# Performance work log

Measured on AMD Instinct MI355X. Metric: run time of the kernel, lower is better.

## Reference

```python
import jax, jax.numpy as jnp
import numpy as np

LEAK = 0.2
EPS = 1e-8


def _mod_conv(x, style, weight):
    # x: [B,C,H,W], style: [B,C], weight: [O,C,k,k]
    b, c, h, w = x.shape
    o, _, k, _ = weight.shape
    # per-sample modulation + demodulation (StyleGAN2 style)
    wmod = weight[None] * (style[:, None, :, None, None] + 1.0)  # [B,O,C,k,k]
    d = jax.lax.rsqrt(jnp.sum(wmod * wmod, axis=(2, 3, 4), keepdims=True) + EPS)
    wmod = wmod * d
    pad = (k - 1) // 2  # same padding for stride=1, dilation=1
    xg = x.reshape(1, b * c, h, w)
    wg = wmod.reshape(b * o, c, k, k)
    y = jax.lax.conv_general_dilated(
        xg, wg, window_strides=(1, 1), padding=[(pad, pad), (pad, pad)],
        dimension_numbers=('NCHW', 'OIHW', 'NCHW'), feature_group_count=b)
    return y.reshape(b, o, h, w)


def setup_inputs() -> dict:
    key = jax.random.key(0)
    ks = jax.random.split(key, 8)
    B, LAT, CIN, F, H, W = 8, 512, 256, 256, 64, 64
    K = 3
    kaiming = lambda k, shape, fan_in: jax.random.normal(k, shape, jnp.float32) * np.sqrt(2.0 / fan_in)
    return {
        'x': jax.random.normal(ks[0], (B, CIN, H, W), jnp.float32),
        'istyle': jax.random.normal(ks[1], (B, LAT), jnp.float32),
        'ws1': jax.random.normal(ks[2], (CIN, LAT), jnp.float32) * (1.0 / np.sqrt(LAT)),
        'bs1': jnp.zeros((CIN,), jnp.float32),
        'conv1_w': kaiming(ks[3], (F, CIN, K, K), CIN * K * K),
        'ws2': jax.random.normal(ks[4], (F, LAT), jnp.float32) * (1.0 / np.sqrt(LAT)),
        'bs2': jnp.zeros((F,), jnp.float32),
        'conv2_w': kaiming(ks[5], (F, F, K, K), F * K * K),
    }


def reference(x, istyle, ws1, bs1, conv1_w, ws2, bs2, conv2_w):
    b, c, h, w = x.shape
    # bilinear upsample x2, align_corners=False (half-pixel centers)
    x = jax.image.resize(x, (b, c, 2 * h, 2 * w), method='bilinear')
    s1 = istyle @ ws1.T + bs1
    x = _mod_conv(x, s1, conv1_w)
    x = jax.nn.leaky_relu(x, LEAK)
    s2 = istyle @ ws2.T + bs2
    x = _mod_conv(x, s2, conv2_w)
    return jax.nn.leaky_relu(x, LEAK)
```

## Files before the change

### kernel.cpp

```cpp
#include <hip/hip_runtime.h>

typedef __bf16 bf16x8 __attribute__((ext_vector_type(8)));
typedef float f32x4 __attribute__((ext_vector_type(4)));


__global__ void style_kernel(const float* __restrict__ istyle,
                             const float* __restrict__ ws1, const float* __restrict__ bs1,
                             const float* __restrict__ ws2, const float* __restrict__ bs2,
                             float* __restrict__ sbuf) {
    int b = blockIdx.x;
    int which = blockIdx.y;
    int c = threadIdx.x;
    const float* ws = which ? ws2 : ws1;
    const float* bs = which ? bs2 : bs1;
    __shared__ float st[512];
    for (int i = threadIdx.x; i < 512; i += 256) st[i] = istyle[b * 512 + i];
    __syncthreads();
    float acc = bs[c];
    const float* wr = ws + (size_t)c * 512;
    for (int l = 0; l < 512; ++l) acc += st[l] * wr[l];
    sbuf[((size_t)which * 8 + b) * 256 + c] = acc;
}

__global__ void modw_kernel(const float* __restrict__ w, const float* __restrict__ s,
                            __bf16* __restrict__ wm) {
    int b = blockIdx.x >> 8;
    int o = blockIdx.x & 255;
    int c = threadIdx.x;
    float sm = s[(size_t)b * 256 + c] + 1.0f;
    float v[9];
    float ss = 0.f;
    const float* wr = w + ((size_t)o * 256 + c) * 9;
#pragma unroll
    for (int t = 0; t < 9; ++t) { v[t] = wr[t] * sm; ss += v[t] * v[t]; }
    __shared__ float red[256];
    red[c] = ss;
    __syncthreads();
    for (int sh = 128; sh > 0; sh >>= 1) {
        if (c < sh) red[c] += red[c + sh];
        __syncthreads();
    }
    float d = rsqrtf(red[0] + 1e-8f);
#pragma unroll
    for (int t = 0; t < 9; ++t)
        wm[(((size_t)(b * 256 + o) * 9 + t) * 256) + c] = (__bf16)(v[t] * d);
}

__global__ void zeropad_kernel(__bf16* __restrict__ xu, __bf16* __restrict__ y1) {
    int p = blockIdx.x;
    int b = blockIdx.y;
    __bf16* buf = blockIdx.z ? y1 : xu;
    int y, x;
    if (p < 130)      { y = 0;           x = p; }
    else if (p < 260) { y = 129;         x = p - 130; }
    else if (p < 388) { y = p - 260 + 1; x = 0; }
    else              { y = p - 388 + 1; x = 129; }
    uint4 z = make_uint4(0, 0, 0, 0);
    *(uint4*)(buf + (((size_t)b * 130 + y) * 130 + x) * 256 + threadIdx.x * 8) = z;
}

__global__ void upsample_kernel(const float* __restrict__ x, __bf16* __restrict__ xu) {
    int ct = blockIdx.x;
    int y  = blockIdx.y;
    int b  = blockIdx.z;
    int c0 = ct * 32;
    __shared__ float up[32 * 132];
    int tid = threadIdx.x;

    int j = y >> 1;
    int y0, y1; float wy0, wy1;
    if (y & 1) { y0 = j; y1 = (j + 1 < 64) ? j + 1 : 63; wy0 = 0.75f; wy1 = 0.25f; }
    else       { y0 = (j - 1 >= 0) ? j - 1 : 0; y1 = j; wy0 = 0.25f; wy1 = 0.75f; }

    int c  = tid >> 3;
    int xs = (tid & 7) * 16;
    const float* row0 = x + ((size_t)(b * 256 + c0 + c) * 64 + y0) * 64;
    const float* row1 = x + ((size_t)(b * 256 + c0 + c) * 64 + y1) * 64;
#pragma unroll
    for (int k = 0; k < 16; ++k) {
        int xo = xs + k;
        int i = xo >> 1;
        int x0, x1; float wx0, wx1;
        if (xo & 1) { x0 = i; x1 = (i + 1 < 64) ? i + 1 : 63; wx0 = 0.75f; wx1 = 0.25f; }
        else        { x0 = (i - 1 >= 0) ? i - 1 : 0; x1 = i; wx0 = 0.25f; wx1 = 0.75f; }
        float v0 = wx0 * row0[x0] + wx1 * row0[x1];
        float v1 = wx0 * row1[x0] + wx1 * row1[x1];
        up[c * 132 + xo] = wy0 * v0 + wy1 * v1;
    }
    __syncthreads();
    int xo = tid >> 1, half = tid & 1;
    union { __bf16 v[8]; uint4 u; } pk;
#pragma unroll
    for (int g = 0; g < 2; ++g) {
#pragma unroll
        for (int i = 0; i < 8; ++i)
            pk.v[i] = (__bf16)up[(half * 16 + g * 8 + i) * 132 + xo];
        *(uint4*)(xu + (((size_t)(b * 130) + y + 1) * 130 + xo + 1) * 256 + c0 + half * 16 + g * 8) = pk.u;
    }
}

template <int PHASE>
__global__ __launch_bounds__(256, 3) void conv_kernel(
    const __bf16* __restrict__ in,
    const __bf16* __restrict__ wm,
    float* __restrict__ outf,
    __bf16* __restrict__ outb) {
    __shared__ __bf16 Al[128 * 64];
    __shared__ __bf16 Bl[128 * 64];
    const int tid   = threadIdx.x;
    const int bid   = blockIdx.x;
    const int swz   = (bid & 7) * 256 + (bid >> 3);
    const int b     = swz >> 8;
    const int bx    = swz & 255;
    const int yrow  = bx >> 1;
    const int mtile = bx & 1;
    const int om    = mtile * 128;
    const int lane  = tid & 63;
    const int wv    = tid >> 6;
    const int wo    = (wv >> 1) * 64;
    const int wn    = (wv & 1) * 64;
    const int lr    = lane >> 3;
    const int lc    = lane & 7;
    const int swzc  = (lc ^ lr) * 8;
    const int arow  = lane & 15;
    const int cgb   = lane >> 4;

    const size_t wmbase = ((size_t)(b * 256 + om + wv * 32 + lr) * 9) * 256 + swzc;
    const size_t inbase = (size_t)b * 130 * 130 * 256 + (size_t)(wv * 32 + lr) * 256 + swzc;

    f32x4 acc[4][4] = {};

    for (int tap = 0; tap < 9; ++tap) {
        const int ky = tap / 3, kx = tap % 3;
        const size_t inrow = inbase + (size_t)((yrow + ky) * 130 + kx) * 256;
        const size_t wrow  = wmbase + (size_t)tap * 256;
        for (int c0 = 0; c0 < 256; c0 += 64) {
#pragma unroll
            for (int q = 0; q < 4; ++q) {
                __builtin_amdgcn_global_load_lds(
                    (const __attribute__((address_space(1))) unsigned int*)(wm + wrow + (size_t)q * 8 * 9 * 256 + c0),
                    (__attribute__((address_space(3))) unsigned int*)(Al + (wv * 32 + q * 8) * 64),
                    16, 0, 0);
                __builtin_amdgcn_global_load_lds(
                    (const __attribute__((address_space(1))) unsigned int*)(in + inrow + (size_t)q * 8 * 256 + c0),
                    (__attribute__((address_space(3))) unsigned int*)(Bl + (wv * 32 + q * 8) * 64),
                    16, 0, 0);
            }
            __syncthreads();
#pragma unroll
            for (int ks = 0; ks < 2; ++ks) {
                const int cg = ks * 4 + cgb;
                bf16x8 af[4], bfr[4];
#pragma unroll
                for (int i = 0; i < 4; ++i) {
                    int ra = wo + i * 16 + arow;
                    af[i]  = *(const bf16x8*)((const char*)Al + ra * 128 + ((cg ^ (ra & 7)) * 16));
                    int rb = wn + i * 16 + arow;
                    bfr[i] = *(const bf16x8*)((const char*)Bl + rb * 128 + ((cg ^ (rb & 7)) * 16));
                }
#pragma unroll
                for (int i = 0; i < 4; ++i)
#pragma unroll
                    for (int j = 0; j < 4; ++j)
                        acc[i][j] = __builtin_amdgcn_mfma_f32_16x16x32_bf16(af[i], bfr[j], acc[i][j], 0, 0, 0);
            }
            __syncthreads();
        }
    }

#pragma unroll
    for (int i = 0; i < 4; ++i) {
#pragma unroll
        for (int j = 0; j < 4; ++j) {
            int o_base = om + wo + i * 16 + (lane >> 4) * 4;
            int n      = wn + j * 16 + (lane & 15);
            if (PHASE == 1) {
                union { __bf16 v[4]; uint2 u; } pk;
#pragma unroll
                for (int r = 0; r < 4; ++r) {
                    float t = acc[i][j][r];
                    t = (t > 0.f) ? t : 0.2f * t;
                    pk.v[r] = (__bf16)t;
                }
                *(uint2*)(outb + (((size_t)(b * 130) + yrow + 1) * 130 + n + 1) * 256 + o_base) = pk.u;
            } else {
#pragma unroll
                for (int r = 0; r < 4; ++r) {
                    float t = acc[i][j][r];
                    t = (t > 0.f) ? t : 0.2f * t;
                    outf[(((size_t)b * 256 + o_base + r) * 128 + yrow) * 128 + n] = t;
                }
            }
        }
    }
}

extern "C" void kernel_launch(void* const* d_in, const int* in_sizes, int n_in,
                              void* d_out, int out_size, void* d_ws, size_t ws_size,
                              hipStream_t stream) {
    const float* x      = (const float*)d_in[0];
    const float* istyle = (const float*)d_in[1];
    const float* ws1    = (const float*)d_in[2];
    const float* bs1    = (const float*)d_in[3];
    const float* w1     = (const float*)d_in[4];
    const float* ws2    = (const float*)d_in[5];
    const float* bs2    = (const float*)d_in[6];
    const float* w2     = (const float*)d_in[7];
    float* out = (float*)d_out;

    char* ws = (char*)d_ws;
    __bf16* xu_p = (__bf16*)(ws);
    __bf16* y1_p = (__bf16*)(ws + 69222400);
    __bf16* wm   = (__bf16*)(ws + 138444800);
    float*  sbuf = (float*)(ws + 147881984);

    style_kernel<<<dim3(8, 2), 256, 0, stream>>>(istyle, ws1, bs1, ws2, bs2, sbuf);
    zeropad_kernel<<<dim3(516, 8, 2), 32, 0, stream>>>(xu_p, y1_p);
    upsample_kernel<<<dim3(8, 128, 8), 256, 0, stream>>>(x, xu_p);
    modw_kernel<<<dim3(2048), 256, 0, stream>>>(w1, sbuf, wm);
    conv_kernel<1><<<dim3(2048), 256, 0, stream>>>(xu_p, wm, nullptr, y1_p);
    modw_kernel<<<dim3(2048), 256, 0, stream>>>(w2, sbuf + 2048, wm);
    conv_kernel<2><<<dim3(2048), 256, 0, stream>>>(y1_p, wm, out, nullptr);
}
```

Baseline: 418.2 us.

## Enlarge conv tile to 256x256 with double-buffered LDS pipeline

Rewrites the modulated-conv implicit GEMM so each 512-thread block computes all 256 output channels over two image rows (256 pixels), instead of 128x128 tiles. Global-to-LDS loads for the next K-step are double-buffered and interleaved with MFMA phases, using explicit vmcnt waits, barriers and setprio. This targets load latency and redundant input/weight traffic across tiles. In exchange it uses 128KB of LDS per block and only 512 blocks, which reduces occupancy and may leave CUs underfilled.

```diff
diff --git a/kernel.cpp b/kernel.cpp
--- a/kernel.cpp
+++ b/kernel.cpp
@@ -3,6 +3,12 @@
 typedef __bf16 bf16x8 __attribute__((ext_vector_type(8)));
 typedef float f32x4 __attribute__((ext_vector_type(4)));
 
+
+#define GLDS(gsrc, ldst) __builtin_amdgcn_global_load_lds( \
+    (const __attribute__((address_space(1))) unsigned int*)(gsrc), \
+    (__attribute__((address_space(3))) unsigned int*)(ldst), 16, 0, 0)
+
+#define MFMA(a, b, c) __builtin_amdgcn_mfma_f32_16x16x32_bf16((a), (b), (c), 0, 0, 0)
 
 __global__ void style_kernel(const float* __restrict__ istyle,
                              const float* __restrict__ ws1, const float* __restrict__ bs1,
@@ -100,95 +106,173 @@
 }
 
 template <int PHASE>
-__global__ __launch_bounds__(256, 3) void conv_kernel(
+__global__ __launch_bounds__(512, 2) void conv_kernel(
     const __bf16* __restrict__ in,
-    const __bf16* __restrict__ wm,
+    const __bf16* __restrict__ wmall,
     float* __restrict__ outf,
     __bf16* __restrict__ outb) {
-    __shared__ __bf16 Al[128 * 64];
-    __shared__ __bf16 Bl[128 * 64];
-    const int tid   = threadIdx.x;
-    const int bid   = blockIdx.x;
-    const int swz   = (bid & 7) * 256 + (bid >> 3);
-    const int b     = swz >> 8;
-    const int bx    = swz & 255;
-    const int yrow  = bx >> 1;
-    const int mtile = bx & 1;
-    const int om    = mtile * 128;
-    const int lane  = tid & 63;
-    const int wv    = tid >> 6;
-    const int wo    = (wv >> 1) * 64;
-    const int wn    = (wv & 1) * 64;
-    const int lr    = lane >> 3;
-    const int lc    = lane & 7;
-    const int swzc  = (lc ^ lr) * 8;
-    const int arow  = lane & 15;
-    const int cgb   = lane >> 4;
-
-    const size_t wmbase = ((size_t)(b * 256 + om + wv * 32 + lr) * 9) * 256 + swzc;
-    const size_t inbase = (size_t)b * 130 * 130 * 256 + (size_t)(wv * 32 + lr) * 256 + swzc;
-
-    f32x4 acc[4][4] = {};
-
-    for (int tap = 0; tap < 9; ++tap) {
-        const int ky = tap / 3, kx = tap % 3;
-        const size_t inrow = inbase + (size_t)((yrow + ky) * 130 + kx) * 256;
-        const size_t wrow  = wmbase + (size_t)tap * 256;
-        for (int c0 = 0; c0 < 256; c0 += 64) {
-#pragma unroll
-            for (int q = 0; q < 4; ++q) {
-                __builtin_amdgcn_global_load_lds(
-                    (const __attribute__((address_space(1))) unsigned int*)(wm + wrow + (size_t)q * 8 * 9 * 256 + c0),
-                    (__attribute__((address_space(3))) unsigned int*)(Al + (wv * 32 + q * 8) * 64),
-                    16, 0, 0);
-                __builtin_amdgcn_global_load_lds(
-                    (const __attribute__((address_space(1))) unsigned int*)(in + inrow + (size_t)q * 8 * 256 + c0),
-                    (__attribute__((address_space(3))) unsigned int*)(Bl + (wv * 32 + q * 8) * 64),
-                    16, 0, 0);
-            }
-            __syncthreads();
-#pragma unroll
-            for (int ks = 0; ks < 2; ++ks) {
-                const int cg = ks * 4 + cgb;
-                bf16x8 af[4], bfr[4];
-#pragma unroll
-                for (int i = 0; i < 4; ++i) {
-                    int ra = wo + i * 16 + arow;
-                    af[i]  = *(const bf16x8*)((const char*)Al + ra * 128 + ((cg ^ (ra & 7)) * 16));
-                    int rb = wn + i * 16 + arow;
-                    bfr[i] = *(const bf16x8*)((const char*)Bl + rb * 128 + ((cg ^ (rb & 7)) * 16));
-                }
-#pragma unroll
-                for (int i = 0; i < 4; ++i)
-#pragma unroll
-                    for (int j = 0; j < 4; ++j)
-                        acc[i][j] = __builtin_amdgcn_mfma_f32_16x16x32_bf16(af[i], bfr[j], acc[i][j], 0, 0, 0);
-            }
-            __syncthreads();
-        }
-    }
-
-#pragma unroll
-    for (int i = 0; i < 4; ++i) {
+    __shared__ __bf16 sA[2][256 * 64];
+    __shared__ __bf16 sB[2][256 * 64];
+    const int tid  = threadIdx.x;
+    const int bid  = blockIdx.x;
+    const int swz  = (bid & 7) * 64 + (bid >> 3);
+    const int b    = swz >> 6;
+    const int yt   = swz & 63;
+    const int lane = tid & 63;
+    const int wv   = tid >> 6;
+    const int wo   = (wv >> 2) * 128;
+    const int wn   = (wv & 3) * 64;
+    const int arow = lane & 15;
+    const int cgb  = lane >> 4;
+    const int xA0  = (cgb ^ (arow & 7)) * 8;
+    const int xA1  = xA0 ^ 32;
+    const int lr   = lane >> 3;
+    const int lc   = lane & 7;
+    const int swz8 = (lc ^ lr) * 8;
+    const __bf16* wm_b = wmall + (size_t)b * 256 * 2304;
+
+    size_t bOff[4], aOff[4];
+#pragma unroll
+    for (int q = 0; q < 4; ++q) {
+        int r  = q * 64 + wv * 8 + lr;
+        int pr = r >> 7, px = r & 127;
+        bOff[q] = ((size_t)((b * 130 + yt * 2 + pr) * 130 + px)) * 256 + swz8;
+        aOff[q] = (size_t)r * 2304 + swz8;
+    }
+
+    f32x4 acc[8][4] = {};
+    bf16x8 bf[4][2];
+
+#pragma unroll
+    for (int q = 0; q < 4; ++q) {
+        GLDS(in + bOff[q],  &sB[0][(q * 64 + wv * 8) * 64]);
+        GLDS(wm_b + aOff[q], &sA[0][(q * 64 + wv * 8) * 64]);
+    }
+    asm volatile("s_waitcnt vmcnt(0)" ::: "memory");
+    __builtin_amdgcn_s_barrier();
+    asm volatile("" ::: "memory");
+
+    for (int t = 0; t < 36; ++t) {
+        const __bf16* Ac = sA[t & 1];
+        const __bf16* Bc = sB[t & 1];
+        __bf16* An = sA[(t + 1) & 1];
+        __bf16* Bn = sB[(t + 1) & 1];
+        const bool st = (t < 35);
+        const int nt = t + 1;
+        const int ntap = nt >> 2, nc0 = (nt & 3) << 6;
+        const int nky = ntap / 3, nkx = ntap - nky * 3;
+        const size_t boff_t = (size_t)((nky * 130 + nkx) * 256 + nc0);
+        const size_t aoff_t = (size_t)(ntap * 256 + nc0);
+
+#define LOADA(qq, A00, A01, A10, A11)                                        \
+        { const __bf16* ap0 = Ac + (wo + (2*(qq)) * 16 + arow) * 64;         \
+          const __bf16* ap1 = Ac + (wo + (2*(qq)+1) * 16 + arow) * 64;       \
+          A00 = *(const bf16x8*)(ap0 + xA0); A01 = *(const bf16x8*)(ap0 + xA1); \
+          A10 = *(const bf16x8*)(ap1 + xA0); A11 = *(const bf16x8*)(ap1 + xA1); }
+
+#define MFMAQ(M0, M1, A00, A01, A10, A11)                                    \
+        _Pragma("unroll")                                                    \
+        for (int j = 0; j < 4; ++j) {                                        \
+            acc[M0][j] = MFMA(A00, bf[j][0], acc[M0][j]);                    \
+            acc[M0][j] = MFMA(A01, bf[j][1], acc[M0][j]);                    \
+            acc[M1][j] = MFMA(A10, bf[j][0], acc[M1][j]);                    \
+            acc[M1][j] = MFMA(A11, bf[j][1], acc[M1][j]);                    \
+        }
+
+        {
+#pragma unroll
+            for (int j = 0; j < 4; ++j) {
+                const __bf16* bp = Bc + (wn + j * 16 + arow) * 64;
+                bf[j][0] = *(const bf16x8*)(bp + xA0);
+                bf[j][1] = *(const bf16x8*)(bp + xA1);
+            }
+            bf16x8 a00, a01, a10, a11;
+            LOADA(0, a00, a01, a10, a11);
+            if (st) {
+                GLDS(in + bOff[0] + boff_t, &Bn[(0 * 64 + wv * 8) * 64]);
+                GLDS(in + bOff[1] + boff_t, &Bn[(1 * 64 + wv * 8) * 64]);
+            }
+            __builtin_amdgcn_s_barrier();
+            asm volatile("" ::: "memory");
+            __builtin_amdgcn_s_setprio(1);
+            MFMAQ(0, 1, a00, a01, a10, a11);
+            __builtin_amdgcn_s_setprio(0);
+            __builtin_amdgcn_s_barrier();
+            asm volatile("" ::: "memory");
+        }
+        {
+            bf16x8 a00, a01, a10, a11;
+            LOADA(1, a00, a01, a10, a11);
+            if (st) {
+                GLDS(in + bOff[2] + boff_t, &Bn[(2 * 64 + wv * 8) * 64]);
+                GLDS(in + bOff[3] + boff_t, &Bn[(3 * 64 + wv * 8) * 64]);
+            }
+            __builtin_amdgcn_s_barrier();
+            asm volatile("" ::: "memory");
+            __builtin_amdgcn_s_setprio(1);
+            MFMAQ(2, 3, a00, a01, a10, a11);
+            __builtin_amdgcn_s_setprio(0);
+            if (st) { asm volatile("s_waitcnt vmcnt(4)" ::: "memory"); }
+            else    { asm volatile("s_waitcnt vmcnt(0)" ::: "memory"); }
+            __builtin_amdgcn_s_barrier();
+            asm volatile("" ::: "memory");
+        }
+        {
+            bf16x8 a00, a01, a10, a11;
+            LOADA(2, a00, a01, a10, a11);
+            if (st) {
+                GLDS(wm_b + aOff[0] + aoff_t, &An[(0 * 64 + wv * 8) * 64]);
+                GLDS(wm_b + aOff[2] + aoff_t, &An[(2 * 64 + wv * 8) * 64]);
+            }
+            __builtin_amdgcn_s_barrier();
+            asm volatile("" ::: "memory");
+            __builtin_amdgcn_s_setprio(1);
+            MFMAQ(4, 5, a00, a01, a10, a11);
+            __builtin_amdgcn_s_setprio(0);
+            __builtin_amdgcn_s_barrier();
+            asm volatile("" ::: "memory");
+        }
+        {
+            bf16x8 a00, a01, a10, a11;
+            LOADA(3, a00, a01, a10, a11);
+            if (st) {
+                GLDS(wm_b + aOff[1] + aoff_t, &An[(1 * 64 + wv * 8) * 64]);
+                GLDS(wm_b + aOff[3] + aoff_t, &An[(3 * 64 + wv * 8) * 64]);
+            }
+            __builtin_amdgcn_s_barrier();
+            asm volatile("" ::: "memory");
+            __builtin_amdgcn_s_setprio(1);
+            MFMAQ(6, 7, a00, a01, a10, a11);
+            __builtin_amdgcn_s_setprio(0);
+            if (st) { asm volatile("s_waitcnt vmcnt(2)" ::: "memory"); }
+            __builtin_amdgcn_s_barrier();
+            asm volatile("" ::: "memory");
+        }
+#undef LOADA
+#undef MFMAQ
+    }
+
+#pragma unroll
+    for (int m = 0; m < 8; ++m) {
 #pragma unroll
         for (int j = 0; j < 4; ++j) {
-            int o_base = om + wo + i * 16 + (lane >> 4) * 4;
+            int o_base = wo + m * 16 + (lane >> 4) * 4;
             int n      = wn + j * 16 + (lane & 15);
+            int pr = n >> 7, px = n & 127;
             if (PHASE == 1) {
                 union { __bf16 v[4]; uint2 u; } pk;
 #pragma unroll
                 for (int r = 0; r < 4; ++r) {
-                    float t = acc[i][j][r];
-                    t = (t > 0.f) ? t : 0.2f * t;
-                    pk.v[r] = (__bf16)t;
+                    float v = acc[m][j][r];
+                    pk.v[r] = (__bf16)((v > 0.f) ? v : 0.2f * v);
                 }
-                *(uint2*)(outb + (((size_t)(b * 130) + yrow + 1) * 130 + n + 1) * 256 + o_base) = pk.u;
+                *(uint2*)(outb + (((size_t)(b * 130) + yt * 2 + pr + 1) * 130 + px + 1) * 256 + o_base) = pk.u;
             } else {
 #pragma unroll
                 for (int r = 0; r < 4; ++r) {
-                    float t = acc[i][j][r];
-                    t = (t > 0.f) ? t : 0.2f * t;
-                    outf[(((size_t)b * 256 + o_base + r) * 128 + yrow) * 128 + n] = t;
+                    float v = acc[m][j][r];
+                    v = (v > 0.f) ? v : 0.2f * v;
+                    outf[((size_t)(b * 256 + o_base + r) * 128 + yt * 2 + pr) * 128 + px] = v;
                 }
             }
         }
@@ -218,7 +302,7 @@
     zeropad_kernel<<<dim3(516, 8, 2), 32, 0, stream>>>(xu_p, y1_p);
     upsample_kernel<<<dim3(8, 128, 8), 256, 0, stream>>>(x, xu_p);
     modw_kernel<<<dim3(2048), 256, 0, stream>>>(w1, sbuf, wm);
-    conv_kernel<1><<<dim3(2048), 256, 0, stream>>>(xu_p, wm, nullptr, y1_p);
+    conv_kernel<1><<<dim3(512), 512, 0, stream>>>(xu_p, wm, nullptr, y1_p);
     modw_kernel<<<dim3(2048), 256, 0, stream>>>(w2, sbuf + 2048, wm);
-    conv_kernel<2><<<dim3(2048), 256, 0, stream>>>(y1_p, wm, out, nullptr);
-}
+    conv_kernel<2><<<dim3(512), 512, 0, stream>>>(y1_p, wm, out, nullptr);
+}
```

New measurement: 397.7 us. -4.9%, faster.
